# Performance work log

Hardware: AMD Instinct MI355X
Metric: run time of the kernel (lower is better)

The kernel has to match this reference:

```python
import math
import jax, jax.numpy as jnp
import numpy as np

B, S, H, NH, BS, R = 2, 4096, 1024, 16, 64, 3
HD = H // NH          # 64 head dim
L = S // BS           # 64 blocks
PEN = -10000.0


def _make_rand_attn():
    # data-independent random block plan (like HF bigbird, seeded numpy),
    # per head, per middle query block: R random key blocks excluding
    # global blocks (0, L-1) and the sliding window (i-1, i, i+1)
    rng = np.random.RandomState(42)
    ra = np.zeros((NH, L - 2, R), dtype=np.int64)
    for h in range(NH):
        for i in range(1, L - 1):
            choices = np.array([j for j in range(L) if j not in (0, i - 1, i, i + 1, L - 1)])
            ra[h, i - 1] = rng.choice(choices, R, replace=False)
    return ra


def setup_inputs():
    key = jax.random.key(0)
    ks = jax.random.split(key, 8)
    sc = 1.0 / math.sqrt(H)
    return {
        "Q": jax.random.normal(ks[0], (B, S, H), jnp.float32),
        "K": jax.random.normal(ks[1], (B, S, H), jnp.float32),
        "V": jax.random.normal(ks[2], (B, S, H), jnp.float32),
        "mask": jnp.ones((B, S), jnp.float32),
        "Wq": jax.random.normal(ks[3], (H, H), jnp.float32) * sc,
        "bq": jnp.zeros((H,), jnp.float32),
        "Wk": jax.random.normal(ks[4], (H, H), jnp.float32) * sc,
        "bk": jnp.zeros((H,), jnp.float32),
        "Wv": jax.random.normal(ks[5], (H, H), jnp.float32) * sc,
        "bv": jnp.zeros((H,), jnp.float32),
        "rand_attn": jnp.asarray(_make_rand_attn()),
    }


def _forward(Q, K, V, mask, Wq, bq, Wk, bk, Wv, bv, rand_attn):
    rsd = 1.0 / math.sqrt(HD)
    sm = lambda x: jax.nn.softmax(x, axis=-1)

    def proj(x, W, b):  # torch Linear: x @ W^T + b, then split heads
        return (x @ W.T + b).reshape(B, S, NH, HD).transpose(0, 2, 1, 3)

    q = proj(Q, Wq, bq)  # [B,NH,S,HD]
    k = proj(K, Wk, bk)
    v = proj(V, Wv, bv)
    qb = q.reshape(B, NH, L, BS, HD)
    kb = k.reshape(B, NH, L, BS, HD)
    vb = v.reshape(B, NH, L, BS, HD)

    # ---- masks (derived from padding mask, as in HF create_masks_...) ----
    blocked = mask.reshape(B, L, BS)
    from_mask = mask[:, None, :, None]   # [B,1,S,1]
    to_mask = mask[:, None, None, :]     # [B,1,1,S]
    exp_to = jnp.concatenate([blocked[:, 1:-3], blocked[:, 2:-2], blocked[:, 3:-1]], axis=2)  # [B,L-4,3BS]
    band_mask = jnp.einsum('blq,blk->blqk', blocked[:, 2:-2], exp_to)[:, None]  # [B,1,L-4,BS,3BS]

    ra = jnp.broadcast_to(rand_attn[None], (B, NH, L - 2, R))
    bidx = jnp.arange(B)[:, None, None, None]
    hidx = jnp.arange(NH)[None, :, None, None]
    gk = kb[bidx, hidx, ra].reshape(B, NH, L - 2, R * BS, HD)  # gathered random key blocks
    gv = vb[bidx, hidx, ra].reshape(B, NH, L - 2, R * BS, HD)
    rm = blocked[bidx, ra].reshape(B, NH, L - 2, R * BS)
    rand_mask = jnp.einsum('blq,bhlk->bhlqk', blocked[:, 1:-1], rm)  # [B,NH,L-2,BS,R*BS]

    # ---- first block: dense attention over all keys ----
    p1 = jnp.einsum('bhqd,bhkd->bhqk', qb[:, :, 0], k) * rsd + (1.0 - to_mask) * PEN
    ctx_first = jnp.einsum('bhqk,bhkd->bhqd', sm(p1), v)

    # ---- second block: global(0) + window(1,2) + last + random ----
    k2 = jnp.concatenate([kb[:, :, 0], kb[:, :, 1], kb[:, :, 2], kb[:, :, -1], gk[:, :, 0]], axis=2)
    v2 = jnp.concatenate([vb[:, :, 0], vb[:, :, 1], vb[:, :, 2], vb[:, :, -1], gv[:, :, 0]], axis=2)
    p2 = jnp.einsum('bhqd,bhkd->bhqk', qb[:, :, 1], k2) * rsd
    seq_pad2 = jnp.concatenate([to_mask[..., :3 * BS], to_mask[..., -BS:],
                                jnp.ones((B, 1, 1, R * BS), mask.dtype)], axis=3)
    rand_pad2 = jnp.concatenate([jnp.ones((B, NH, BS, 4 * BS), mask.dtype), rand_mask[:, :, 0]], axis=3)
    p2 = p2 + (1.0 - jnp.minimum(seq_pad2, rand_pad2)) * PEN
    ctx_second = jnp.einsum('bhqk,bhkd->bhqd', sm(p2), v2)

    # ---- middle blocks: band (3 sliding) + random + 2 global ----
    exp_k = jnp.concatenate([kb[:, :, 1:-3], kb[:, :, 2:-2], kb[:, :, 3:-1]], axis=3)  # [B,NH,L-4,3BS,HD]
    exp_v = jnp.concatenate([vb[:, :, 1:-3], vb[:, :, 2:-2], vb[:, :, 3:-1]], axis=3)
    mq = qb[:, :, 2:-2]
    inner = jnp.einsum('bhlqd,bhlkd->bhlqk', mq, exp_k) * rsd + (1.0 - band_mask) * PEN
    randp = jnp.einsum('bhlqd,bhlkd->bhlqk', mq, gk[:, :, 1:-1]) * rsd + (1.0 - rand_mask[:, :, 1:-1]) * PEN
    firstp = jnp.einsum('bhlqd,bhkd->bhlqk', mq, kb[:, :, 0]) * rsd + (1.0 - to_mask[:, :, :, None, :BS]) * PEN
    lastp = jnp.einsum('bhlqd,bhkd->bhlqk', mq, kb[:, :, -1]) * rsd + (1.0 - to_mask[:, :, :, None, -BS:]) * PEN
    w = sm(jnp.concatenate([firstp, inner, randp, lastp], axis=-1))  # [B,NH,L-4,BS,(5+R)*BS]
    ctx_mid = jnp.einsum('bhlqk,bhlkd->bhlqd', w[..., BS:4 * BS], exp_v)
    ctx_mid += jnp.einsum('bhlqk,bhlkd->bhlqd', w[..., 4 * BS:(4 + R) * BS], gv[:, :, 1:-1])
    ctx_mid += jnp.einsum('bhlqk,bhkd->bhlqd', w[..., :BS], vb[:, :, 0])
    ctx_mid += jnp.einsum('bhlqk,bhkd->bhlqd', w[..., -BS:], vb[:, :, -1])

    # ---- second-to-last block ----
    k3 = jnp.concatenate([kb[:, :, 0], kb[:, :, -3], kb[:, :, -2], kb[:, :, -1], gk[:, :, -1]], axis=2)
    v3 = jnp.concatenate([vb[:, :, 0], vb[:, :, -3], vb[:, :, -2], vb[:, :, -1], gv[:, :, -1]], axis=2)
    p3 = jnp.einsum('bhqd,bhkd->bhqk', qb[:, :, -2], k3) * rsd
    seq_pad3 = jnp.concatenate([to_mask[..., :BS], to_mask[..., -3 * BS:],
                                jnp.ones((B, 1, 1, R * BS), mask.dtype)], axis=3)
    rand_pad3 = jnp.concatenate([jnp.ones((B, NH, BS, 4 * BS), mask.dtype), rand_mask[:, :, -1]], axis=3)
    p3 = p3 + (1.0 - jnp.minimum(seq_pad3, rand_pad3)) * PEN
    ctx_seclast = jnp.einsum('bhqk,bhkd->bhqd', sm(p3), v3)

    # ---- last block: dense attention over all keys ----
    p4 = jnp.einsum('bhqd,bhkd->bhqk', qb[:, :, -1], k) * rsd + (1.0 - to_mask) * PEN
    ctx_last = jnp.einsum('bhqk,bhkd->bhqd', sm(p4), v)

    ctx = jnp.concatenate([ctx_first[:, :, None], ctx_second[:, :, None], ctx_mid,
                           ctx_seclast[:, :, None], ctx_last[:, :, None]], axis=2)
    ctx = ctx.reshape(B, NH, S, HD) * from_mask
    return ctx.transpose(0, 2, 1, 3).reshape(B, S, NH * HD)


def reference(Q, K, V, mask, Wq, bq, Wk, bk, Wv, bv, rand_attn):
    return _forward(Q, K, V, mask, Wq, bq, Wk, bk, Wv, bv, rand_attn)
```

## Files before the change

### kernel.cpp

```cpp
#include <hip/hip_runtime.h>
#include <hip/hip_bf16.h>
#include <stdint.h>

#define BB 2
#define SS 4096
#define HH 1024
#define NHh 16
#define HD 64
#define LL 64
#define BS 64
#define RR 3
#define PENf (-10000.0f)

typedef unsigned int uint;
typedef __attribute__((ext_vector_type(8))) short bf16x8;
typedef __attribute__((ext_vector_type(4))) float f32x4;

__device__ __forceinline__ ushort f2bf(float f) {
    union { float f; uint u; } v; v.f = f;
    uint u = v.u;
    return (ushort)((u + 0x7fffu + ((u >> 16) & 1u)) >> 16);
}
__device__ __forceinline__ uint pack_bf(float a, float b) {
    uint r;
    asm("v_cvt_pk_bf16_f32 %0, %1, %2" : "=v"(r) : "v"(a), "v"(b));
    return r;
}
__device__ __forceinline__ uint scale_pair(uint w) {
    float lo = __uint_as_float(w << 16) * 0.125f;
    float hi = __uint_as_float(w & 0xffff0000u) * 0.125f;
    return pack_bf(lo, hi);
}
__device__ __forceinline__ uint4 scale4(uint4 w) {
    uint4 o;
    o.x = scale_pair(w.x); o.y = scale_pair(w.y);
    o.z = scale_pair(w.z); o.w = scale_pair(w.w);
    return o;
}
__device__ __forceinline__ void async16(const ushort* g, ushort* l) {
    __builtin_amdgcn_global_load_lds((const __attribute__((address_space(1))) uint*)g,
                                     (__attribute__((address_space(3))) uint*)l,
                                     16, 0, 0);
}

__global__ __launch_bounds__(256)
void cvt_kernel(const float* __restrict__ Xq, const float* __restrict__ Xk,
                const float* __restrict__ Xv, const float* __restrict__ Wq,
                const float* __restrict__ Wk, const float* __restrict__ Wv,
                ushort* __restrict__ Xbf, ushort* __restrict__ Wbf)
{
    const size_t XTOT = (size_t)3 * BB * SS * HH;
    const uint u = blockIdx.x * 256 + threadIdx.x;
    const size_t e = (size_t)u * 8;
    const float* src; ushort* dst;
    if (e < XTOT) {
        const int zz = (int)(e >> 23);
        src = (zz == 0 ? Xq : zz == 1 ? Xk : Xv) + (e & ((1u << 23) - 1));
        dst = Xbf + e;
    } else {
        const size_t e2 = e - XTOT;
        const int zz = (int)(e2 >> 20);
        src = (zz == 0 ? Wq : zz == 1 ? Wk : Wv) + (e2 & ((1u << 20) - 1));
        dst = Wbf + e2;
    }
    float4 a = ((const float4*)src)[0];
    float4 c = ((const float4*)src)[1];
    uint4 o;
    o.x = pack_bf(a.x, a.y); o.y = pack_bf(a.z, a.w);
    o.z = pack_bf(c.x, c.y); o.w = pack_bf(c.z, c.w);
    *(uint4*)dst = o;
}

__global__ __launch_bounds__(512)
void gemm6_kernel(const ushort* __restrict__ Xbf, const ushort* __restrict__ Wbf,
                  const float* __restrict__ bq, const float* __restrict__ bk,
                  const float* __restrict__ bv,
                  ushort* __restrict__ qb, ushort* __restrict__ kb,
                  ushort* __restrict__ vbT)
{
    __shared__ __align__(16) ushort smem6[49152];

    const int z = blockIdx.z;
    const ushort* Ag = Xbf + (size_t)z * ((size_t)BB * SS * HH);
    const ushort* Bg = Wbf + (size_t)z * (HH * HH);
    const float* bias = (z == 0) ? bq : (z == 1) ? bk : bv;
    const bool zv = (z == 2);

    const int tid = threadIdx.x;
    const int m0 = blockIdx.x * 128;
    const int n0 = blockIdx.y * 256;
    const int wave = tid >> 6;
    const int lane = tid & 63;
    const int l15 = lane & 15;
    const int quad = lane >> 4;
    const int wr = wave >> 2;
    const int wc = wave & 3;

    f32x4 acc[4][4];
#pragma unroll
    for (int i = 0; i < 4; ++i)
#pragma unroll
        for (int j = 0; j < 4; ++j) acc[i][j] = (f32x4){0.f, 0.f, 0.f, 0.f};

    const int trow = tid >> 2;
    const int tcol = ((tid & 3) ^ ((tid >> 3) & 3)) * 8;
    const ushort* Ath  = Ag + (size_t)(m0 + trow) * HH + tcol;
    const ushort* Bth  = Bg + (size_t)(n0 + trow) * HH + tcol;
    const ushort* Bth2 = Bth + (size_t)128 * HH;
    const int sl8 = (quad ^ ((l15 >> 1) & 3)) * 8;

#define STAGE6(kt_)                                                    \
    do {                                                               \
        const int k0_ = (kt_) * 32;                                    \
        const int sb_ = ((kt_) & 3) * 12288 + wave * 512;              \
        async16(Ath + k0_,  smem6 + sb_);                              \
        async16(Bth + k0_,  smem6 + sb_ + 4096);                       \
        async16(Bth2 + k0_, smem6 + sb_ + 8192);                       \
    } while (0)

#define TB6(kt_, VM_, DOSTAGE_)                                                     \
    do {                                                                            \
        const int bo_ = ((kt_) & 3) * 12288;                                        \
        asm volatile("s_waitcnt vmcnt(" #VM_ ")" ::: "memory");                     \
        __builtin_amdgcn_s_barrier();                                               \
        __builtin_amdgcn_sched_barrier(0);                                          \
        const ushort* Ab_ = smem6 + bo_;                                            \
        const ushort* Bb_ = smem6 + bo_ + 4096;                                     \
        bf16x8 af_[4], bf_[4];                                                      \
        _Pragma("unroll")                                                           \
        for (int mt = 0; mt < 4; ++mt)                                              \
            af_[mt] = *(const bf16x8*)(Ab_ + (wr * 64 + mt * 16 + l15) * 32 + sl8); \
        _Pragma("unroll")                                                           \
        for (int nt = 0; nt < 4; ++nt)                                              \
            bf_[nt] = *(const bf16x8*)(Bb_ + (wc * 64 + nt * 16 + l15) * 32 + sl8); \
        if (DOSTAGE_) STAGE6((kt_) + 3);                                            \
        __builtin_amdgcn_s_setprio(1);                                              \
        if (zv) {                                                                   \
            _Pragma("unroll")                                                       \
            for (int i = 0; i < 4; ++i)                                             \
                _Pragma("unroll")                                                   \
                for (int j = 0; j < 4; ++j)                                         \
                    acc[i][j] = __builtin_amdgcn_mfma_f32_16x16x32_bf16(            \
                        af_[i], bf_[j], acc[i][j], 0, 0, 0);                        \
        } else {                                                                    \
            _Pragma("unroll")                                                       \
            for (int i = 0; i < 4; ++i)                                             \
                _Pragma("unroll")                                                   \
                for (int j = 0; j < 4; ++j)                                         \
                    acc[i][j] = __builtin_amdgcn_mfma_f32_16x16x32_bf16(            \
                        bf_[i], af_[j], acc[i][j], 0, 0, 0);                        \
        }                                                                           \
        __builtin_amdgcn_s_setprio(0);                                              \
    } while (0)

    STAGE6(0); STAGE6(1); STAGE6(2);

    for (int k4 = 0; k4 < 28; k4 += 4) {
        TB6(k4 + 0, 6, 1);
        TB6(k4 + 1, 6, 1);
        TB6(k4 + 2, 6, 1);
        TB6(k4 + 3, 6, 1);
    }
    TB6(28, 6, 1);
    TB6(29, 6, 0);
    TB6(30, 3, 0);
    TB6(31, 0, 0);
#undef TB6
#undef STAGE6

    if (!zv) {
        ushort* outp = (z == 0) ? qb : kb;
#pragma unroll
        for (int wt = 0; wt < 4; ++wt) {
            const int nb = n0 + wc * 64 + wt * 16 + quad * 4;
            const float4 b4 = *(const float4*)&bias[nb];
            const int nh = nb >> 6;
            const int hd = nb & 63;
#pragma unroll
            for (int xt = 0; xt < 4; ++xt) {
                const int m = m0 + wr * 64 + xt * 16 + l15;
                const int bgl = m >> 12, s = m & 4095;
                uint2 pk;
                pk.x = pack_bf(acc[wt][xt][0] + b4.x, acc[wt][xt][1] + b4.y);
                pk.y = pack_bf(acc[wt][xt][2] + b4.z, acc[wt][xt][3] + b4.w);
                *(uint2*)&outp[((size_t)((bgl << 4) | nh) * SS + s) * HD + hd] = pk;
            }
        }
    } else {
        __syncthreads();
        ushort* stg = smem6;
        const int bgl = m0 >> 12;
#pragma unroll
        for (int nt = 0; nt < 4; ++nt) {
            const int n_local = wc * 64 + nt * 16 + l15;
            const float bn = bias[n0 + n_local];
#pragma unroll
            for (int mt = 0; mt < 4; ++mt) {
                const int m_base = wr * 64 + mt * 16 + quad * 4;
                uint2 pk;
                pk.x = pack_bf(acc[mt][nt][0] + bn, acc[mt][nt][1] + bn);
                pk.y = pack_bf(acc[mt][nt][2] + bn, acc[mt][nt][3] + bn);
                *(uint2*)(stg + n_local * 136 + m_base) = pk;
            }
        }
        __syncthreads();
        const int n_row = tid >> 1;
        const int half = tid & 1;
        const int n = n0 + n_row;
        const int nh = n >> 6, hd = n & 63;
        const uint4* src = (const uint4*)(stg + n_row * 136 + half * 64);
        uint4* dst = (uint4*)(vbT + ((size_t)((bgl << 4) | nh) * HD + hd) * SS
                              + (m0 & 4095) + half * 64);
#pragma unroll
        for (int jj = 0; jj < 8; ++jj) dst[jj] = src[jj];
    }
}

__global__ __launch_bounds__(256)
void proj3_kernel(const float* __restrict__ Xq, const float* __restrict__ Xk,
                  const float* __restrict__ Xv,
                  const float* __restrict__ Wq, const float* __restrict__ Wk,
                  const float* __restrict__ Wv,
                  const float* __restrict__ bq, const float* __restrict__ bk,
                  const float* __restrict__ bv,
                  ushort* __restrict__ qb, ushort* __restrict__ kb,
                  ushort* __restrict__ vbT)
{
    __shared__ __align__(16) ushort smem[128 * 136];
    ushort* As = smem;
    ushort* Bs = smem + 128 * 40;

    const int z = blockIdx.z;
    const float* X    = (z == 0) ? Xq : (z == 1) ? Xk : Xv;
    const float* W    = (z == 0) ? Wq : (z == 1) ? Wk : Wv;
    const float* bias = (z == 0) ? bq : (z == 1) ? bk : bv;

    const int tid = threadIdx.x;
    const int m0 = blockIdx.x * 128;
    const int n0 = blockIdx.y * 128;
    const int wave = tid >> 6;
    const int lane = tid & 63;
    const int l15 = lane & 15;
    const int quad = lane >> 4;
    const int wr = wave >> 1, wc = wave & 1;

    f32x4 acc[4][4];
#pragma unroll
    for (int mt = 0; mt < 4; ++mt)
#pragma unroll
        for (int nt = 0; nt < 4; ++nt) acc[mt][nt] = (f32x4){0.f, 0.f, 0.f, 0.f};

    const int srow = tid >> 1;
    const int shalf = tid & 1;
    const float* xp = X + (size_t)(m0 + srow) * HH + shalf * 16;
    const float* wp = W + (size_t)(n0 + srow) * HH + shalf * 16;
    ushort* asw = As + srow * 40 + shalf * 16;
    ushort* bsw = Bs + srow * 40 + shalf * 16;

    for (int k0 = 0; k0 < HH; k0 += 32) {
        float4 a0 = *(const float4*)(xp + k0);
        float4 a1 = *(const float4*)(xp + k0 + 4);
        float4 a2 = *(const float4*)(xp + k0 + 8);
        float4 a3 = *(const float4*)(xp + k0 + 12);
        float4 b0 = *(const float4*)(wp + k0);
        float4 b1 = *(const float4*)(wp + k0 + 4);
        float4 b2 = *(const float4*)(wp + k0 + 8);
        float4 b3 = *(const float4*)(wp + k0 + 12);
        __syncthreads();
        uint4 pa, pb;
        pa.x = pack_bf(a0.x, a0.y); pa.y = pack_bf(a0.z, a0.w);
        pa.z = pack_bf(a1.x, a1.y); pa.w = pack_bf(a1.z, a1.w);
        *(uint4*)asw = pa;
        pa.x = pack_bf(a2.x, a2.y); pa.y = pack_bf(a2.z, a2.w);
        pa.z = pack_bf(a3.x, a3.y); pa.w = pack_bf(a3.z, a3.w);
        *(uint4*)(asw + 8) = pa;
        pb.x = pack_bf(b0.x, b0.y); pb.y = pack_bf(b0.z, b0.w);
        pb.z = pack_bf(b1.x, b1.y); pb.w = pack_bf(b1.z, b1.w);
        *(uint4*)bsw = pb;
        pb.x = pack_bf(b2.x, b2.y); pb.y = pack_bf(b2.z, b2.w);
        pb.z = pack_bf(b3.x, b3.y); pb.w = pack_bf(b3.z, b3.w);
        *(uint4*)(bsw + 8) = pb;
        __syncthreads();

        bf16x8 af[4], bfr[4];
#pragma unroll
        for (int mt = 0; mt < 4; ++mt)
            af[mt] = *(const bf16x8*)(As + (wr * 64 + mt * 16 + l15) * 40 + quad * 8);
#pragma unroll
        for (int nt = 0; nt < 4; ++nt)
            bfr[nt] = *(const bf16x8*)(Bs + (wc * 64 + nt * 16 + l15) * 40 + quad * 8);
#pragma unroll
        for (int mt = 0; mt < 4; ++mt)
#pragma unroll
            for (int nt = 0; nt < 4; ++nt)
                acc[mt][nt] = __builtin_amdgcn_mfma_f32_16x16x32_bf16(af[mt], bfr[nt], acc[mt][nt], 0, 0, 0);
    }

    if (z < 2) {
        ushort* outp = (z == 0) ? qb : kb;
#pragma unroll
        for (int nt = 0; nt < 4; ++nt) {
            const int n = n0 + wc * 64 + nt * 16 + l15;
            const float bn = bias[n];
            const int nh = n >> 6, hd = n & 63;
#pragma unroll
            for (int mt = 0; mt < 4; ++mt) {
#pragma unroll
                for (int rr = 0; rr < 4; ++rr) {
                    const int m = m0 + wr * 64 + mt * 16 + quad * 4 + rr;
                    const int bgl = m >> 12, s = m & 4095;
                    outp[((size_t)((bgl << 4) | nh) * SS + s) * HD + hd] = f2bf(acc[mt][nt][rr] + bn);
                }
            }
        }
    } else {
        __syncthreads();
        ushort* stg = smem;
#pragma unroll
        for (int nt = 0; nt < 4; ++nt) {
            const int n_local = wc * 64 + nt * 16 + l15;
            const float bn = bias[n0 + n_local];
#pragma unroll
            for (int mt = 0; mt < 4; ++mt) {
                const int m_base = wr * 64 + mt * 16 + quad * 4;
                uint2 pk;
                pk.x = pack_bf(acc[mt][nt][0] + bn, acc[mt][nt][1] + bn);
                pk.y = pack_bf(acc[mt][nt][2] + bn, acc[mt][nt][3] + bn);
                *(uint2*)(stg + n_local * 136 + m_base) = pk;
            }
        }
        __syncthreads();
        const int n_row = tid >> 1;
        const int half = tid & 1;
        const int n = n0 + n_row;
        const int nh = n >> 6, hd = n & 63;
        const int bgl = m0 >> 12;
        const int sbase = (m0 & 4095) + half * 64;
        const uint4* src = (const uint4*)(stg + n_row * 136 + half * 64);
        uint4* dst = (uint4*)(vbT + ((size_t)((bgl << 4) | nh) * HD + hd) * SS + sbase);
#pragma unroll
        for (int j = 0; j < 8; ++j) dst[j] = src[j];
    }
}

__global__ __launch_bounds__(256)
void attn_kernel(const ushort* __restrict__ qg, const ushort* __restrict__ kg,
                 const ushort* __restrict__ vTg,
                 const float* __restrict__ mask, const int* __restrict__ rand_attn,
                 float* __restrict__ out, float* __restrict__ partO,
                 float* __restrict__ partML)
{
    __shared__ __align__(16) ushort qs_ps[64][72];
    __shared__ __align__(16) ushort ks2[2][2][64][32];
    __shared__ __align__(16) ushort vs2[2][2][64][32];
    __shared__ __align__(16) float qm_s[64];
    __shared__ __align__(16) float km_s[2][64];

    const int tid = threadIdx.x;
    const int wid = blockIdx.x;
    const int bh = wid / 78;
    const int r = wid - bh * 78;
    const int b = bh >> 4, h = bh & 15;

    int i, nkb;
    int kbl[8], pfl[8];
    bool dense;
    int part = 0, which = 0;
    if (r < 62) {
        dense = false;
        i = r + 1;
        const int* ra = rand_attn + ((size_t)h * (LL - 2) + (i - 1)) * RR;
        if (i == 1) {
            kbl[0] = 0; kbl[1] = 1; kbl[2] = 2; kbl[3] = LL - 1;
            kbl[4] = ra[0]; kbl[5] = ra[1]; kbl[6] = ra[2]; kbl[7] = 0;
            pfl[0] = pfl[1] = pfl[2] = pfl[3] = 0;
            pfl[4] = pfl[5] = pfl[6] = 1; pfl[7] = 0;
            nkb = 7;
        } else if (i == LL - 2) {
            kbl[0] = 0; kbl[1] = LL - 3; kbl[2] = LL - 2; kbl[3] = LL - 1;
            kbl[4] = ra[0]; kbl[5] = ra[1]; kbl[6] = ra[2]; kbl[7] = 0;
            pfl[0] = pfl[1] = pfl[2] = pfl[3] = 0;
            pfl[4] = pfl[5] = pfl[6] = 1; pfl[7] = 0;
            nkb = 7;
        } else {
            kbl[0] = 0;      pfl[0] = 0;
            kbl[1] = i - 1;  pfl[1] = 1;
            kbl[2] = i;      pfl[2] = 1;
            kbl[3] = i + 1;  pfl[3] = 1;
            kbl[4] = LL - 1; pfl[4] = 0;
            kbl[5] = ra[0]; kbl[6] = ra[1]; kbl[7] = ra[2];
            pfl[5] = pfl[6] = pfl[7] = 1;
            nkb = 8;
        }
    } else {
        dense = true;
        const int r2 = r - 62;
        which = r2 >> 3;
        part = r2 & 7;
        i = which ? (LL - 1) : 0;
        nkb = 8;
#pragma unroll
        for (int j = 0; j < 8; ++j) { kbl[j] = part * 8 + j; pfl[j] = 0; }
    }

    const int lane = tid & 63;
    const int wave = tid >> 6;
    const int l15 = lane & 15;
    const int quad = lane >> 4;
    const int srow = lane >> 2;
    const int p8s = (((lane & 3) ^ ((srow >> 1) & 3))) * 8;
    const ushort* kgb = kg + (size_t)bh * SS * HD;
    const ushort* vgb = vTg + (size_t)bh * HD * SS;

#define STAGE_KV(kb_, bp)                                                        \
    do {                                                                         \
        const size_t krow = (size_t)((kb_) * BS + wave * 16 + srow) * HD;        \
        async16(kgb + krow + p8s,      &ks2[bp][0][wave * 16][0]);               \
        async16(kgb + krow + 32 + p8s, &ks2[bp][1][wave * 16][0]);               \
        const size_t vrow = (size_t)(wave * 16 + srow) * SS + (kb_) * BS;        \
        async16(vgb + vrow + p8s,      &vs2[bp][0][wave * 16][0]);               \
        async16(vgb + vrow + 32 + p8s, &vs2[bp][1][wave * 16][0]);               \
    } while (0)

    {
        const int row = tid >> 2;
        const int c0 = (tid & 3) * 16;
        const ushort* src = qg + ((size_t)bh * SS + i * BS + row) * HD + c0;
        uint4 w0 = *(const uint4*)src;
        uint4 w1 = *(const uint4*)(src + 8);
        *(uint4*)&qs_ps[row][c0] = scale4(w0);
        *(uint4*)&qs_ps[row][c0 + 8] = scale4(w1);
        if (tid < 64) qm_s[tid] = mask[(size_t)b * SS + i * BS + tid];
    }
    STAGE_KV(kbl[0], 0);
    if (tid < 64) km_s[0][tid] = mask[(size_t)b * SS + kbl[0] * BS + tid];
    __syncthreads();

    bf16x8 aq[2];
    aq[0] = *(const bf16x8*)&qs_ps[wave * 16 + l15][quad * 8];
    aq[1] = *(const bf16x8*)&qs_ps[wave * 16 + l15][32 + quad * 8];
    const float qm = qm_s[wave * 16 + l15];

    const int sqz = (quad ^ ((l15 >> 1) & 3)) * 8;

    float mrow = -1e30f, lrow = 0.0f;
    f32x4 accO[4];
#pragma unroll
    for (int dt = 0; dt < 4; ++dt) accO[dt] = (f32x4){0.f, 0.f, 0.f, 0.f};

    for (int it = 0; it < nkb; ++it) {
        const int cur = it & 1;
        if (it + 1 < nkb) {
            STAGE_KV(kbl[it + 1], cur ^ 1);
            if (tid < 64) km_s[cur ^ 1][tid] = mask[(size_t)b * SS + kbl[it + 1] * BS + tid];
        }
        const int pf = pfl[it];

        f32x4 sc[4];
#pragma unroll
        for (int nt = 0; nt < 4; ++nt) sc[nt] = (f32x4){0.f, 0.f, 0.f, 0.f};
#pragma unroll
        for (int c = 0; c < 2; ++c) {
#pragma unroll
            for (int nt = 0; nt < 4; ++nt) {
                bf16x8 af = *(const bf16x8*)&ks2[cur][c][nt * 16 + l15][sqz];
                sc[nt] = __builtin_amdgcn_mfma_f32_16x16x32_bf16(af, aq[c], sc[nt], 0, 0, 0);
            }
        }

        float p[4][4];
        float bm = -1e30f;
#pragma unroll
        for (int nt = 0; nt < 4; ++nt) {
            const float4 km4 = *(const float4*)&km_s[cur][nt * 16 + quad * 4];
            const float kmv[4] = {km4.x, km4.y, km4.z, km4.w};
#pragma unroll
            for (int rr = 0; rr < 4; ++rr) {
                const float pm = pf ? (qm * kmv[rr]) : kmv[rr];
                const float sv = sc[nt][rr] + (1.0f - pm) * PENf;
                p[nt][rr] = sv;
                bm = fmaxf(bm, sv);
            }
        }
        bm = fmaxf(bm, __shfl_xor(bm, 16));
        bm = fmaxf(bm, __shfl_xor(bm, 32));
        if (!__all(bm - mrow <= 8.0f)) {
            const float mn = fmaxf(mrow, bm);
            const float alpha = __expf(mrow - mn);
            mrow = mn;
            float a4[4];
#pragma unroll
            for (int rr = 0; rr < 4; ++rr) a4[rr] = __shfl(alpha, quad * 4 + rr, 64);
#pragma unroll
            for (int dt = 0; dt < 4; ++dt) {
#pragma unroll
                for (int rr = 0; rr < 4; ++rr) accO[dt][rr] *= a4[rr];
            }
            lrow *= alpha;
        }
        float ls = 0.0f;
#pragma unroll
        for (int nt = 0; nt < 4; ++nt)
#pragma unroll
            for (int rr = 0; rr < 4; ++rr) {
                p[nt][rr] = __expf(p[nt][rr] - mrow);
                ls += p[nt][rr];
            }
        ls += __shfl_xor(ls, 16);
        ls += __shfl_xor(ls, 32);
        lrow += ls;

#pragma unroll
        for (int nt = 0; nt < 4; ++nt) {
            uint2 pk;
            pk.x = pack_bf(p[nt][0], p[nt][1]);
            pk.y = pack_bf(p[nt][2], p[nt][3]);
            *(uint2*)&qs_ps[wave * 16 + l15][nt * 16 + quad * 4] = pk;
        }

#pragma unroll
        for (int c = 0; c < 2; ++c) {
            bf16x8 ap = *(const bf16x8*)&qs_ps[wave * 16 + l15][c * 32 + quad * 8];
#pragma unroll
            for (int dt = 0; dt < 4; ++dt) {
                bf16x8 bvf = *(const bf16x8*)&vs2[cur][c][dt * 16 + l15][sqz];
                accO[dt] = __builtin_amdgcn_mfma_f32_16x16x32_bf16(ap, bvf, accO[dt], 0, 0, 0);
            }
        }

        if (it + 1 < nkb) __syncthreads();
    }
#undef STAGE_KV

    if (!dense) {
#pragma unroll
        for (int rr = 0; rr < 4; ++rr) {
            const int qloc = quad * 4 + rr;
            const float lq = __shfl(lrow, qloc, 64);
            const float inv = qm_s[wave * 16 + qloc] / lq;
#pragma unroll
            for (int dt = 0; dt < 4; ++dt) {
                const int d = dt * 16 + l15;
                out[((size_t)b * SS + i * BS + wave * 16 + qloc) * HH + h * HD + d] = accO[dt][rr] * inv;
            }
        }
    } else {
        const int slot = (bh * 2 + which) * 8 + part;
        float* po = partO + (size_t)slot * 4096;
#pragma unroll
        for (int rr = 0; rr < 4; ++rr) {
            const int qrow = wave * 16 + quad * 4 + rr;
#pragma unroll
            for (int dt = 0; dt < 4; ++dt) {
                const int d = dt * 16 + l15;
                po[qrow * 64 + d] = accO[dt][rr];
            }
        }
        if (lane < 16) {
            partML[slot * 128 + wave * 16 + lane] = mrow;
            partML[slot * 128 + 64 + wave * 16 + lane] = lrow;
        }
    }
}

__global__ __launch_bounds__(64)
void combine_kernel(const float* __restrict__ partO, const float* __restrict__ partML,
                    const float* __restrict__ mask, float* __restrict__ out)
{
    const int g4 = blockIdx.x;
    const int g = g4 >> 2;
    const int bh = g >> 1, which = g & 1;
    const int b = bh >> 4, h = bh & 15;
    const int i = which ? (LL - 1) : 0;
    const int t = threadIdx.x;
    const int row = ((g4 & 3) << 4) | (t >> 2);
    const int d0 = (t & 3) * 16;
    const int base = g * 8;

    float mp[8], lp[8];
    float M = -1e30f;
#pragma unroll
    for (int p = 0; p < 8; ++p) {
        mp[p] = partML[(base + p) * 128 + row];
        lp[p] = partML[(base + p) * 128 + 64 + row];
        M = fmaxf(M, mp[p]);
    }
    float L = 0.0f, w[8];
#pragma unroll
    for (int p = 0; p < 8; ++p) { w[p] = __expf(mp[p] - M); L += lp[p] * w[p]; }

    float4 o[4];
#pragma unroll
    for (int j = 0; j < 4; ++j) o[j] = make_float4(0.f, 0.f, 0.f, 0.f);
#pragma unroll
    for (int p = 0; p < 8; ++p) {
        const float* po = partO + (size_t)(base + p) * 4096 + row * 64 + d0;
#pragma unroll
        for (int j = 0; j < 4; ++j) {
            float4 v = *(const float4*)(po + j * 4);
            o[j].x = fmaf(w[p], v.x, o[j].x);
            o[j].y = fmaf(w[p], v.y, o[j].y);
            o[j].z = fmaf(w[p], v.z, o[j].z);
            o[j].w = fmaf(w[p], v.w, o[j].w);
        }
    }
    const float fm = mask[(size_t)b * SS + i * BS + row];
    const float inv = fm / L;
    float* dst = out + ((size_t)b * SS + i * BS + row) * HH + h * HD + d0;
#pragma unroll
    for (int j = 0; j < 4; ++j) {
        float4 v;
        v.x = o[j].x * inv; v.y = o[j].y * inv;
        v.z = o[j].z * inv; v.w = o[j].w * inv;
        *(float4*)(dst + j * 4) = v;
    }
}

extern "C" void kernel_launch(void* const* d_in, const int* in_sizes, int n_in,
                              void* d_out, int out_size, void* d_ws, size_t ws_size,
                              hipStream_t stream) {
    (void)in_sizes; (void)n_in; (void)out_size;
    const float* Q    = (const float*)d_in[0];
    const float* K    = (const float*)d_in[1];
    const float* V    = (const float*)d_in[2];
    const float* mask = (const float*)d_in[3];
    const float* Wq   = (const float*)d_in[4];
    const float* bq   = (const float*)d_in[5];
    const float* Wk   = (const float*)d_in[6];
    const float* bk   = (const float*)d_in[7];
    const float* Wv   = (const float*)d_in[8];
    const float* bv   = (const float*)d_in[9];
    const int*   ra   = (const int*)d_in[10];
    float* out = (float*)d_out;

    const size_t qkv = (size_t)BB * NHh * SS * HD;
    ushort* qb  = (ushort*)d_ws;
    ushort* kb  = qb + qkv;
    ushort* vbT = kb + qkv;
    float* partO  = (float*)(vbT + qkv);
    float* partML = partO + (size_t)512 * 4096;
    ushort* Xbf = (ushort*)(partML + (size_t)512 * 128);
    ushort* Wbf = Xbf + 3 * qkv;
    const size_t need = (size_t)((char*)(Wbf + (size_t)3 * HH * HH) - (char*)d_ws);

    if (ws_size >= need) {
        cvt_kernel<<<13824, 256, 0, stream>>>(Q, K, V, Wq, Wk, Wv, Xbf, Wbf);
        gemm6_kernel<<<dim3(64, 4, 3), 512, 0, stream>>>(Xbf, Wbf, bq, bk, bv, qb, kb, vbT);
    } else {
        proj3_kernel<<<dim3(64, 8, 3), 256, 0, stream>>>(Q, K, V, Wq, Wk, Wv, bq, bk, bv,
                                                         qb, kb, vbT);
    }
    attn_kernel<<<dim3(BB * NHh * 78), 256, 0, stream>>>(qb, kb, vbT, mask, ra,
                                                         out, partO, partML);
    combine_kernel<<<dim3(BB * NHh * 2 * 4), 64, 0, stream>>>(partO, partML, mask, out);
}
```

Before: 280.9 us.

## Switch GEMM to 3-stage LDS ring and use exp2-domain softmax with max3

The projection GEMM moves from a 4-buffer, prefetch-distance-3 LDS ring to a 3-buffer, distance-2 ring. This cuts shared memory per block, which may allow more resident blocks, at the cost of less latency hiding. The attention kernel folds log2(e) into the score and mask penalty, uses raw v_exp_f32 and v_max3_f32, and scales the lazy-rescale threshold to match. The K/V staging addresses are also simplified into precomputed base pointers. The merge kernel uses exp2 on max values that are now in the log2 domain.

```diff
diff --git a/kernel.cpp b/kernel.cpp
--- a/kernel.cpp
+++ b/kernel.cpp
@@ -11,6 +11,8 @@
 #define BS 64
 #define RR 3
 #define PENf (-10000.0f)
+#define L2E 1.44269504f
+#define PENL (-14426.9504f)
 
 typedef unsigned int uint;
 typedef __attribute__((ext_vector_type(8))) short bf16x8;
@@ -24,6 +26,16 @@
 __device__ __forceinline__ uint pack_bf(float a, float b) {
     uint r;
     asm("v_cvt_pk_bf16_f32 %0, %1, %2" : "=v"(r) : "v"(a), "v"(b));
+    return r;
+}
+__device__ __forceinline__ float fexp2(float x) {
+    float r;
+    asm("v_exp_f32 %0, %1" : "=v"(r) : "v"(x));
+    return r;
+}
+__device__ __forceinline__ float fmax3(float a, float b, float c) {
+    float r;
+    asm("v_max3_f32 %0, %1, %2, %3" : "=v"(r) : "v"(a), "v"(b), "v"(c));
     return r;
 }
 __device__ __forceinline__ uint scale_pair(uint w) {
@@ -78,7 +90,7 @@
                   ushort* __restrict__ qb, ushort* __restrict__ kb,
                   ushort* __restrict__ vbT)
 {
-    __shared__ __align__(16) ushort smem6[49152];
+    __shared__ __align__(16) ushort smem6[36864];
 
     const int z = blockIdx.z;
     const ushort* Ag = Xbf + (size_t)z * ((size_t)BB * SS * HH);
@@ -109,18 +121,18 @@
     const ushort* Bth2 = Bth + (size_t)128 * HH;
     const int sl8 = (quad ^ ((l15 >> 1) & 3)) * 8;
 
-#define STAGE6(kt_)                                                    \
+#define STAGE6(kt_, bb_)                                               \
     do {                                                               \
         const int k0_ = (kt_) * 32;                                    \
-        const int sb_ = ((kt_) & 3) * 12288 + wave * 512;              \
+        const int sb_ = (bb_) * 12288 + wave * 512;                    \
         async16(Ath + k0_,  smem6 + sb_);                              \
         async16(Bth + k0_,  smem6 + sb_ + 4096);                       \
         async16(Bth2 + k0_, smem6 + sb_ + 8192);                       \
     } while (0)
 
-#define TB6(kt_, VM_, DOSTAGE_)                                                     \
+#define TB6(kt_, bpi_, VM_, DOSTAGE_, sbf_)                                         \
     do {                                                                            \
-        const int bo_ = ((kt_) & 3) * 12288;                                        \
+        const int bo_ = (bpi_) * 12288;                                             \
         asm volatile("s_waitcnt vmcnt(" #VM_ ")" ::: "memory");                     \
         __builtin_amdgcn_s_barrier();                                               \
         __builtin_amdgcn_sched_barrier(0);                                          \
@@ -133,7 +145,7 @@
         _Pragma("unroll")                                                           \
         for (int nt = 0; nt < 4; ++nt)                                              \
             bf_[nt] = *(const bf16x8*)(Bb_ + (wc * 64 + nt * 16 + l15) * 32 + sl8); \
-        if (DOSTAGE_) STAGE6((kt_) + 3);                                            \
+        if (DOSTAGE_) STAGE6((kt_) + 2, sbf_);                                      \
         __builtin_amdgcn_s_setprio(1);                                              \
         if (zv) {                                                                   \
             _Pragma("unroll")                                                       \
@@ -153,18 +165,15 @@
         __builtin_amdgcn_s_setprio(0);                                              \
     } while (0)
 
-    STAGE6(0); STAGE6(1); STAGE6(2);
-
-    for (int k4 = 0; k4 < 28; k4 += 4) {
-        TB6(k4 + 0, 6, 1);
-        TB6(k4 + 1, 6, 1);
-        TB6(k4 + 2, 6, 1);
-        TB6(k4 + 3, 6, 1);
-    }
-    TB6(28, 6, 1);
-    TB6(29, 6, 0);
-    TB6(30, 3, 0);
-    TB6(31, 0, 0);
+    STAGE6(0, 0); STAGE6(1, 1);
+
+    for (int k3 = 0; k3 < 30; k3 += 3) {
+        TB6(k3 + 0, 0, 3, 1, 2);
+        TB6(k3 + 1, 1, 3, 1, 0);
+        TB6(k3 + 2, 2, 3, 1, 1);
+    }
+    TB6(30, 0, 3, 0, 0);
+    TB6(31, 1, 0, 0, 0);
 #undef TB6
 #undef STAGE6
 
@@ -411,15 +420,18 @@
     const int p8s = (((lane & 3) ^ ((srow >> 1) & 3))) * 8;
     const ushort* kgb = kg + (size_t)bh * SS * HD;
     const ushort* vgb = vTg + (size_t)bh * HD * SS;
-
-#define STAGE_KV(kb_, bp)                                                        \
-    do {                                                                         \
-        const size_t krow = (size_t)((kb_) * BS + wave * 16 + srow) * HD;        \
-        async16(kgb + krow + p8s,      &ks2[bp][0][wave * 16][0]);               \
-        async16(kgb + krow + 32 + p8s, &ks2[bp][1][wave * 16][0]);               \
-        const size_t vrow = (size_t)(wave * 16 + srow) * SS + (kb_) * BS;        \
-        async16(vgb + vrow + p8s,      &vs2[bp][0][wave * 16][0]);               \
-        async16(vgb + vrow + 32 + p8s, &vs2[bp][1][wave * 16][0]);               \
+    const ushort* kl = kgb + (size_t)(wave * 16 + srow) * HD + p8s;
+    const ushort* vl = vgb + (size_t)(wave * 16 + srow) * SS + p8s;
+    const float* maskb = mask + (size_t)b * SS;
+
+#define STAGE_KV(kb_, bp)                                                \
+    do {                                                                 \
+        const ushort* ka_ = kl + ((size_t)(kb_) << 12);                  \
+        async16(ka_,      &ks2[bp][0][wave * 16][0]);                    \
+        async16(ka_ + 32, &ks2[bp][1][wave * 16][0]);                    \
+        const ushort* va_ = vl + ((uint)(kb_) << 6);                     \
+        async16(va_,      &vs2[bp][0][wave * 16][0]);                    \
+        async16(va_ + 32, &vs2[bp][1][wave * 16][0]);                    \
     } while (0)
 
     {
@@ -430,10 +442,10 @@
         uint4 w1 = *(const uint4*)(src + 8);
         *(uint4*)&qs_ps[row][c0] = scale4(w0);
         *(uint4*)&qs_ps[row][c0 + 8] = scale4(w1);
-        if (tid < 64) qm_s[tid] = mask[(size_t)b * SS + i * BS + tid];
+        if (tid < 64) qm_s[tid] = maskb[i * BS + tid];
     }
     STAGE_KV(kbl[0], 0);
-    if (tid < 64) km_s[0][tid] = mask[(size_t)b * SS + kbl[0] * BS + tid];
+    if (tid < 64) km_s[0][tid] = maskb[kbl[0] * BS + tid];
     __syncthreads();
 
     bf16x8 aq[2];
@@ -452,9 +464,8 @@
         const int cur = it & 1;
         if (it + 1 < nkb) {
             STAGE_KV(kbl[it + 1], cur ^ 1);
-            if (tid < 64) km_s[cur ^ 1][tid] = mask[(size_t)b * SS + kbl[it + 1] * BS + tid];
-        }
-        const int pf = pfl[it];
+            if (tid < 64) km_s[cur ^ 1][tid] = maskb[kbl[it + 1] * BS + tid];
+        }
 
         f32x4 sc[4];
 #pragma unroll
@@ -468,25 +479,32 @@
             }
         }
 
+        const float qmEff = pfl[it] ? qm : 1.0f;
         float p[4][4];
-        float bm = -1e30f;
 #pragma unroll
         for (int nt = 0; nt < 4; ++nt) {
             const float4 km4 = *(const float4*)&km_s[cur][nt * 16 + quad * 4];
             const float kmv[4] = {km4.x, km4.y, km4.z, km4.w};
 #pragma unroll
             for (int rr = 0; rr < 4; ++rr) {
-                const float pm = pf ? (qm * kmv[rr]) : kmv[rr];
-                const float sv = sc[nt][rr] + (1.0f - pm) * PENf;
-                p[nt][rr] = sv;
-                bm = fmaxf(bm, sv);
-            }
-        }
+                const float pm = qmEff * kmv[rr];
+                const float w  = fmaf(pm, -PENL, PENL);
+                p[nt][rr] = fmaf(sc[nt][rr], L2E, w);
+            }
+        }
+        float bm = fmax3(p[0][0], p[0][1], p[0][2]);
+        bm = fmax3(bm, p[0][3], p[1][0]);
+        bm = fmax3(bm, p[1][1], p[1][2]);
+        bm = fmax3(bm, p[1][3], p[2][0]);
+        bm = fmax3(bm, p[2][1], p[2][2]);
+        bm = fmax3(bm, p[2][3], p[3][0]);
+        bm = fmax3(bm, p[3][1], p[3][2]);
+        bm = fmaxf(bm, p[3][3]);
         bm = fmaxf(bm, __shfl_xor(bm, 16));
         bm = fmaxf(bm, __shfl_xor(bm, 32));
-        if (!__all(bm - mrow <= 8.0f)) {
+        if (!__all(bm - mrow <= 11.5409f)) {
             const float mn = fmaxf(mrow, bm);
-            const float alpha = __expf(mrow - mn);
+            const float alpha = fexp2(mrow - mn);
             mrow = mn;
             float a4[4];
 #pragma unroll
@@ -503,7 +521,7 @@
         for (int nt = 0; nt < 4; ++nt)
 #pragma unroll
             for (int rr = 0; rr < 4; ++rr) {
-                p[nt][rr] = __expf(p[nt][rr] - mrow);
+                p[nt][rr] = fexp2(p[nt][rr] - mrow);
                 ls += p[nt][rr];
             }
         ls += __shfl_xor(ls, 16);
@@ -587,7 +605,7 @@
     }
     float L = 0.0f, w[8];
 #pragma unroll
-    for (int p = 0; p < 8; ++p) { w[p] = __expf(mp[p] - M); L += lp[p] * w[p]; }
+    for (int p = 0; p < 8; ++p) { w[p] = fexp2(mp[p] - M); L += lp[p] * w[p]; }
 
     float4 o[4];
 #pragma unroll
```

After: 292.8 us. 1.04x slower.
